# Kernel tuning notes

Hardware: AMD Instinct MI355X
Metric: run time of the kernel (lower is better)

The kernel has to match this reference:

```python
import jax, jax.numpy as jnp
import numpy as np

DIM = 128
HEADS = 4
WS = 8  # window size
HEAD_DIM = DIM // HEADS
LOG100 = float(np.log(100.0))


def _cpb_constants(ws):
    # log-spaced relative coordinates table, shape [(2ws-1)^2, 2]
    rng = np.arange(-(ws - 1), ws, dtype=np.float32)
    table = np.stack(np.meshgrid(rng, rng, indexing='ij'), axis=-1)  # [2ws-1,2ws-1,2]
    table = table / (ws - 1)
    table = table * 8.0
    table = np.sign(table) * np.log2(np.abs(table) + 1.0) / np.log2(8.0)
    table = table.reshape(-1, 2)
    # relative position index, shape [ws^2, ws^2]
    coords = np.stack(np.meshgrid(np.arange(ws), np.arange(ws), indexing='ij'), axis=0).reshape(2, -1)
    rel = coords[:, :, None] - coords[:, None, :]  # [2, ws^2, ws^2]
    idx = (rel[0] + ws - 1) * (2 * ws - 1) + (rel[1] + ws - 1)
    return jnp.asarray(table), jnp.asarray(idx.astype(np.int32))


def setup_inputs() -> dict:
    key = jax.random.key(0)
    ks = jax.random.split(key, 10)
    B, H, W = 16, 128, 128
    nW = (H // WS) * (W // WS)
    return {
        'x': jax.random.normal(ks[0], (B, H, W, DIM), jnp.float32),
        'mask': jnp.zeros((nW, WS * WS, WS * WS), jnp.float32),
        'qkv_w': jax.random.normal(ks[1], (DIM, 3 * DIM), jnp.float32) * 0.02,
        'q_bias': jax.random.normal(ks[2], (DIM,), jnp.float32) * 0.02,
        'v_bias': jax.random.normal(ks[3], (DIM,), jnp.float32) * 0.02,
        'logit_scale': jnp.full((HEADS,), float(np.log(10.0)), jnp.float32),
        'cpb_w1': jax.random.normal(ks[4], (2, 512), jnp.float32) * 0.02,
        'cpb_b1': jax.random.normal(ks[5], (512,), jnp.float32) * 0.02,
        'cpb_w2': jax.random.normal(ks[6], (512, HEADS), jnp.float32) * 0.02,
        'proj_w': jax.random.normal(ks[7], (DIM, DIM), jnp.float32) * 0.02,
        'proj_b': jax.random.normal(ks[8], (DIM,), jnp.float32) * 0.02,
        'height': 128,
        'width': 128,
    }


def reference(x, mask, qkv_w, q_bias, v_bias, logit_scale, cpb_w1, cpb_b1, cpb_w2, proj_w, proj_b, height, width):
    B = x.shape[0]
    N = WS * WS
    wh, ww = height // WS, width // WS
    nW = wh * ww

    # QKV projection, K has no bias
    qkv_b = jnp.concatenate([q_bias, jnp.zeros_like(q_bias), v_bias])
    qkv = x @ qkv_w + qkv_b  # [B,H,W,3*DIM]

    # fused window partition -> [3, B*nW, heads, N, head_dim]
    qkv = qkv.reshape(B, wh, WS, ww, WS, 3, HEADS, HEAD_DIM)
    qkv = jnp.transpose(qkv, (5, 0, 1, 3, 6, 2, 4, 7)).reshape(3, B * nW, HEADS, N, HEAD_DIM)
    q, k, v = qkv[0], qkv[1], qkv[2]

    # cosine attention with clamped learnable temperature
    q = q / jnp.maximum(jnp.linalg.norm(q, axis=-1, keepdims=True), 1e-12)
    k = k / jnp.maximum(jnp.linalg.norm(k, axis=-1, keepdims=True), 1e-12)
    scale = jnp.exp(jnp.minimum(logit_scale, LOG100))  # [heads]
    attn = jnp.einsum('whqd,whkd->whqk', q, k) * scale[None, :, None, None]

    # continuous relative position bias via small MLP
    table, idx = _cpb_constants(WS)
    bias_tab = jax.nn.relu(table @ cpb_w1 + cpb_b1) @ cpb_w2  # [(2ws-1)^2, heads]
    bias = 16.0 * jax.nn.sigmoid(bias_tab[idx])  # [N, N, heads]
    attn = attn + jnp.transpose(bias, (2, 0, 1))[None]

    # shifted-window mask
    attn = attn.reshape(B, nW, HEADS, N, N) + mask[None, :, None, :, :]
    attn = jax.nn.softmax(attn.reshape(B * nW, HEADS, N, N), axis=-1)

    out = jnp.einsum('whqk,whkd->whqd', attn, v)  # [B*nW, heads, N, head_dim]

    # fused window reverse -> [B, H, W, DIM]
    out = out.reshape(B, wh, ww, HEADS, WS, WS, HEAD_DIM)
    out = jnp.transpose(out, (0, 1, 4, 2, 5, 3, 6)).reshape(B, height, width, DIM)

    return out @ proj_w + proj_b
```

## Files before the change

kernel.cpp:

```cpp
#include <hip/hip_runtime.h>

typedef unsigned short u16;
typedef __bf16 bf16x8 __attribute__((ext_vector_type(8)));
typedef float f32x4 __attribute__((ext_vector_type(4)));
typedef int i32x4 __attribute__((ext_vector_type(4)));
typedef i32x4 i32x4_a __attribute__((may_alias));
typedef bf16x8 bf16x8_a __attribute__((may_alias));

__device__ __forceinline__ float bf2f(u16 u) {
  union { unsigned int i; float f; } c;
  c.i = ((unsigned int)u) << 16;
  return c.f;
}
__device__ __forceinline__ u16 f2bf(float f) {
  union { __bf16 h; u16 u; } c;
  c.h = (__bf16)f;
  return c.u;
}
__device__ __forceinline__ float gld(const void* p, int i, int isbf) {
  return isbf ? bf2f(((const u16*)p)[i]) : ((const float*)p)[i];
}
__device__ __forceinline__ int sw(int row, int col, int rs) {
  return row * rs + ((((col >> 3) ^ (row & 7)) << 3) | (col & 7));
}

#define WQKVT_OFF 0
#define PWT_OFF   98304
#define QKVB_OFF  131072
#define BIAS_OFF  132608
#define SCALE_OFF 198144
#define PB_OFF    198160
#define FLAG_OFF  198672

__global__ void swin_detect(const unsigned int* __restrict__ xw,
                            unsigned int* __restrict__ flag) {
  int t = threadIdx.x;
  int cnt = 0;
  for (int i = 0; i < 8; i++) {
    unsigned int w = xw[t * 8 + i];
    unsigned int lo = w & 0xffffu;
    unsigned int e = (lo >> 7) & 0xffu;
    if ((e >= 0x70u && e <= 0x82u) || lo == 0u) cnt++;
  }
  cnt += __shfl_xor(cnt, 1);
  cnt += __shfl_xor(cnt, 2);
  cnt += __shfl_xor(cnt, 4);
  cnt += __shfl_xor(cnt, 8);
  cnt += __shfl_xor(cnt, 16);
  cnt += __shfl_xor(cnt, 32);
  if (t == 0) *flag = (cnt >= 256) ? 1u : 0u;
}

__global__ void swin_setup(const void* __restrict__ qkv_w, const void* __restrict__ q_bias,
                           const void* __restrict__ v_bias, const void* __restrict__ ls,
                           const void* __restrict__ cpb_w1, const void* __restrict__ cpb_b1,
                           const void* __restrict__ cpb_w2, const void* __restrict__ proj_w,
                           const void* __restrict__ proj_b, char* __restrict__ ws) {
  const int b = blockIdx.x, t = threadIdx.x;
  const int isbf = (int)*(const unsigned int*)(ws + FLAG_OFF);
  u16* wqkvT = (u16*)(ws + WQKVT_OFF);
  u16* pwT = (u16*)(ws + PWT_OFF);
  float* qkvb = (float*)(ws + QKVB_OFF);
  float* bias16 = (float*)(ws + BIAS_OFF);
  float* scalef = (float*)(ws + SCALE_OFF);
  float* pbf = (float*)(ws + PB_OFF);

  if (b < 128) {
    for (int c = t; c < 384; c += 256)
      wqkvT[c * 128 + b] = f2bf(gld(qkv_w, b * 384 + c, isbf));
  } else if (b < 256) {
    int r = b - 128;
    if (t < 128) pwT[t * 128 + r] = f2bf(gld(proj_w, r * 128 + t, isbf));
  } else if (b == 256) {
    for (int o = t; o < 384; o += 256) {
      float v = 0.f;
      if (o < 128) v = gld(q_bias, o, isbf);
      else if (o >= 256) v = gld(v_bias, o - 256, isbf);
      qkvb[o] = v;
    }
    if (t < 128) pbf[t] = gld(proj_b, t, isbf);
    if (t < 4) scalef[t] = expf(fminf(gld(ls, t, isbf), 4.60517019f));
  } else {
    __shared__ float w1[1024];
    __shared__ float b1[512];
    __shared__ float w2[2048];
    __shared__ float tab[225][4];
    for (int i = t; i < 1024; i += 256) w1[i] = gld(cpb_w1, i, isbf);
    for (int i = t; i < 512; i += 256) b1[i] = gld(cpb_b1, i, isbf);
    for (int i = t; i < 2048; i += 256) w2[i] = gld(cpb_w2, i, isbf);
    __syncthreads();
    if (t < 225) {
      int i = t / 15, j = t % 15;
      float c0, c1;
      {
        float tt = ((float)(i - 7) / 7.0f) * 8.0f;
        float s = (tt > 0.f) ? 1.f : ((tt < 0.f) ? -1.f : 0.f);
        c0 = s * log2f(fabsf(tt) + 1.f) / 3.0f;
      }
      {
        float tt = ((float)(j - 7) / 7.0f) * 8.0f;
        float s = (tt > 0.f) ? 1.f : ((tt < 0.f) ? -1.f : 0.f);
        c1 = s * log2f(fabsf(tt) + 1.f) / 3.0f;
      }
      float acc[4] = {0.f, 0.f, 0.f, 0.f};
      for (int jj = 0; jj < 512; jj++) {
        float h = fmaxf(c0 * w1[jj] + c1 * w1[512 + jj] + b1[jj], 0.f);
        #pragma unroll
        for (int hh = 0; hh < 4; hh++) acc[hh] += h * w2[jj * 4 + hh];
      }
      #pragma unroll
      for (int hh = 0; hh < 4; hh++) tab[t][hh] = acc[hh];
    }
    __syncthreads();
    for (int e = t; e < 4 * 64 * 64; e += 256) {
      int h = e >> 12, q = (e >> 6) & 63, kk = e & 63;
      int dr = (q >> 3) - (kk >> 3) + 7;
      int dc = (q & 7) - (kk & 7) + 7;
      float v = tab[dr * 15 + dc][h];
      bias16[e] = 16.f / (1.f + expf(-v));
    }
  }
}

#define X_OFF 0
#define Q_OFF 0
#define K_OFF 8192
#define VT_OFF 16384
#define P_OFF 0
#define AO_OFF 0

__global__ __launch_bounds__(512, 4) void swin_main(
    const void* __restrict__ x, const void* __restrict__ mask,
    const char* __restrict__ ws, void* __restrict__ out) {
  __shared__ __align__(16) u16 lds[24576];
  const f32x4 fz = {0.f, 0.f, 0.f, 0.f};

  const u16* wqkvT = (const u16*)(ws + WQKVT_OFF);
  const u16* pwT = (const u16*)(ws + PWT_OFF);
  const float* qkvb = (const float*)(ws + QKVB_OFF);
  const float* bias16 = (const float*)(ws + BIAS_OFF);
  const float* scalef = (const float*)(ws + SCALE_OFF);
  const float* pbf = (const float*)(ws + PB_OFF);
  const int isbf = (int)*(const unsigned int*)(ws + FLAG_OFF);

  const int tid = threadIdx.x;
  const int wid = tid >> 6;
  const int lane = tid & 63;
  const int ln16 = lane & 15;
  const int lq = lane >> 4;
  const int q8 = lq << 3;
  const int mg = wid >> 2;
  const int sub = wid & 3;

  const int wi = blockIdx.x;
  const int b = wi >> 8;
  const int rem = wi & 255;
  const int wy = rem >> 4, wx = rem & 15;
  const int xbase = ((b * 128 + wy * 8) * 128 + wx * 8) * 128;

  if (isbf) {
    const u16* xb = (const u16*)x;
    #pragma unroll
    for (int rep = 0; rep < 2; rep++) {
      int ch = tid + rep * 512;
      int token = ch >> 4, dch = ch & 15;
      int r = token >> 3, c = token & 7;
      i32x4 v = *(const i32x4_a*)(xb + xbase + r * 16384 + c * 128 + dch * 8);
      *(i32x4_a*)(lds + X_OFF + sw(token, dch * 8, 128)) = v;
    }
  } else {
    const float* xf = (const float*)x;
    #pragma unroll
    for (int rep = 0; rep < 2; rep++) {
      int ch = tid + rep * 512;
      int token = ch >> 4, dch = ch & 15;
      int r = token >> 3, c = token & 7;
      const float* src = xf + xbase + r * 16384 + c * 128 + dch * 8;
      union { i32x4 v2[2]; float f[8]; } in;
      in.v2[0] = *(const i32x4_a*)(src);
      in.v2[1] = *(const i32x4_a*)(src + 4);
      union { u16 u[8]; i32x4 v; } o;
      #pragma unroll
      for (int d = 0; d < 8; d++) o.u[d] = f2bf(in.f[d]);
      *(i32x4_a*)(lds + X_OFF + sw(token, dch * 8, 128)) = o.v;
    }
  }
  __syncthreads();

  f32x4 acc1[2][6];
  #pragma unroll
  for (int nt = 0; nt < 6; nt++) {
    float bv = qkvb[96 * sub + 16 * nt + ln16];
    f32x4 ci = {bv, bv, bv, bv};
    acc1[0][nt] = ci;
    acc1[1][nt] = ci;
  }

  #pragma unroll
  for (int ks = 0; ks < 4; ks++) {
    bf16x8 a0 = *(const bf16x8_a*)(lds + X_OFF + sw(32 * mg + ln16, 32 * ks + q8, 128));
    bf16x8 a1 = *(const bf16x8_a*)(lds + X_OFF + sw(32 * mg + 16 + ln16, 32 * ks + q8, 128));
    bf16x8 bb[6];
    #pragma unroll
    for (int nt = 0; nt < 6; nt++)
      bb[nt] = *(const bf16x8_a*)(wqkvT + (96 * sub + 16 * nt + ln16) * 128 + 32 * ks + q8);
    #pragma unroll
    for (int nt = 0; nt < 6; nt++) {
      acc1[0][nt] = __builtin_amdgcn_mfma_f32_16x16x32_bf16(a0, bb[nt], acc1[0][nt], 0, 0, 0);
      acc1[1][nt] = __builtin_amdgcn_mfma_f32_16x16x32_bf16(a1, bb[nt], acc1[1][nt], 0, 0, 0);
    }
  }
  __syncthreads();

  #pragma unroll
  for (int ci = 0; ci < 3; ci++) {
    int n0 = 96 * sub + 32 * ci;
    int type = n0 >> 7;
    int head = (n0 & 127) >> 5;
    int nt0 = 2 * ci, nt1 = nt0 + 1;
    if (type < 2) {
      int base = (type == 0) ? Q_OFF : K_OFF;
      float sh = (type == 0) ? scalef[head] : 1.0f;
      #pragma unroll
      for (int mt = 0; mt < 2; mt++)
        #pragma unroll
        for (int r = 0; r < 4; r++) {
          float x0 = acc1[mt][nt0][r], x1 = acc1[mt][nt1][r];
          float ss = x0 * x0 + x1 * x1;
          ss += __shfl_xor(ss, 1);
          ss += __shfl_xor(ss, 2);
          ss += __shfl_xor(ss, 4);
          ss += __shfl_xor(ss, 8);
          float inv = sh / fmaxf(sqrtf(ss), 1e-12f);
          int row = 32 * mg + 16 * mt + 4 * lq + r;
          lds[base + sw(row, head * 32 + ln16, 128)] = f2bf(x0 * inv);
          lds[base + sw(row, head * 32 + 16 + ln16, 128)] = f2bf(x1 * inv);
        }
    } else {
      #pragma unroll
      for (int mt = 0; mt < 2; mt++)
        #pragma unroll
        for (int r = 0; r < 4; r++) {
          int row = 32 * mg + 16 * mt + 4 * lq + r;
          lds[VT_OFF + sw(head * 32 + ln16, row, 64)] = f2bf(acc1[mt][nt0][r]);
          lds[VT_OFF + sw(head * 32 + 16 + ln16, row, 64)] = f2bf(acc1[mt][nt1][r]);
        }
    }
  }
  __syncthreads();

  const int h = sub;
  bf16x8 qf[2], kf[4];
  #pragma unroll
  for (int mt = 0; mt < 2; mt++)
    qf[mt] = *(const bf16x8_a*)(lds + Q_OFF + sw(32 * mg + 16 * mt + ln16, h * 32 + q8, 128));
  #pragma unroll
  for (int nt = 0; nt < 4; nt++)
    kf[nt] = *(const bf16x8_a*)(lds + K_OFF + sw(16 * nt + ln16, h * 32 + q8, 128));

  const float* brow = bias16 + h * 4096;
  const u16* mk16 = (const u16*)mask;
  const float* mkf = (const float*)mask;
  f32x4 S[2][4];
  #pragma unroll
  for (int mt = 0; mt < 2; mt++)
    #pragma unroll
    for (int nt = 0; nt < 4; nt++)
      #pragma unroll
      for (int r = 0; r < 4; r++) {
        int row = 32 * mg + 16 * mt + 4 * lq + r;
        int col = 16 * nt + ln16;
        int bi = row * 64 + col;
        float mval = isbf ? bf2f(mk16[rem * 4096 + bi]) : mkf[rem * 4096 + bi];
        S[mt][nt][r] = brow[bi] + mval;
      }
  #pragma unroll
  for (int mt = 0; mt < 2; mt++)
    #pragma unroll
    for (int nt = 0; nt < 4; nt++)
      S[mt][nt] = __builtin_amdgcn_mfma_f32_16x16x32_bf16(qf[mt], kf[nt], S[mt][nt], 0, 0, 0);

  #pragma unroll
  for (int mt = 0; mt < 2; mt++)
    #pragma unroll
    for (int r = 0; r < 4; r++) {
      float m = fmaxf(fmaxf(S[mt][0][r], S[mt][1][r]), fmaxf(S[mt][2][r], S[mt][3][r]));
      m = fmaxf(m, __shfl_xor(m, 1));
      m = fmaxf(m, __shfl_xor(m, 2));
      m = fmaxf(m, __shfl_xor(m, 4));
      m = fmaxf(m, __shfl_xor(m, 8));
      float sum = 0.f;
      #pragma unroll
      for (int nt = 0; nt < 4; nt++) {
        float p = __expf(S[mt][nt][r] - m);
        S[mt][nt][r] = p;
        sum += p;
      }
      sum += __shfl_xor(sum, 1);
      sum += __shfl_xor(sum, 2);
      sum += __shfl_xor(sum, 4);
      sum += __shfl_xor(sum, 8);
      float inv = 1.0f / sum;
      #pragma unroll
      for (int nt = 0; nt < 4; nt++) S[mt][nt][r] *= inv;
    }
  __syncthreads();

  #pragma unroll
  for (int mt = 0; mt < 2; mt++)
    #pragma unroll
    for (int nt = 0; nt < 4; nt++)
      #pragma unroll
      for (int r = 0; r < 4; r++) {
        int row = 32 * mg + 16 * mt + 4 * lq + r;
        lds[P_OFF + sw(row, h * 64 + 16 * nt + ln16, 256)] = f2bf(S[mt][nt][r]);
      }
  __syncthreads();
  f32x4 O[2][2];
  O[0][0] = fz; O[0][1] = fz; O[1][0] = fz; O[1][1] = fz;
  #pragma unroll
  for (int ks = 0; ks < 2; ks++) {
    bf16x8 pf[2], vf[2];
    #pragma unroll
    for (int mt = 0; mt < 2; mt++)
      pf[mt] = *(const bf16x8_a*)(lds + P_OFF + sw(32 * mg + 16 * mt + ln16, h * 64 + 32 * ks + q8, 256));
    #pragma unroll
    for (int nt = 0; nt < 2; nt++)
      vf[nt] = *(const bf16x8_a*)(lds + VT_OFF + sw(h * 32 + 16 * nt + ln16, 32 * ks + q8, 64));
    #pragma unroll
    for (int mt = 0; mt < 2; mt++)
      #pragma unroll
      for (int nt = 0; nt < 2; nt++)
        O[mt][nt] = __builtin_amdgcn_mfma_f32_16x16x32_bf16(pf[mt], vf[nt], O[mt][nt], 0, 0, 0);
  }
  __syncthreads();
  #pragma unroll
  for (int mt = 0; mt < 2; mt++)
    #pragma unroll
    for (int nt = 0; nt < 2; nt++)
      #pragma unroll
      for (int r = 0; r < 4; r++) {
        int row = 32 * mg + 16 * mt + 4 * lq + r;
        lds[AO_OFF + sw(row, h * 32 + 16 * nt + ln16, 128)] = f2bf(O[mt][nt][r]);
      }
  __syncthreads();

  float pb0 = pbf[32 * sub + ln16];
  float pb1 = pbf[32 * sub + 16 + ln16];
  f32x4 acc3[2][2];
  {
    f32x4 c0 = {pb0, pb0, pb0, pb0};
    f32x4 c1 = {pb1, pb1, pb1, pb1};
    acc3[0][0] = c0; acc3[0][1] = c1; acc3[1][0] = c0; acc3[1][1] = c1;
  }
  #pragma unroll
  for (int ks = 0; ks < 4; ks++) {
    bf16x8 a0 = *(const bf16x8_a*)(lds + AO_OFF + sw(32 * mg + ln16, 32 * ks + q8, 128));
    bf16x8 a1 = *(const bf16x8_a*)(lds + AO_OFF + sw(32 * mg + 16 + ln16, 32 * ks + q8, 128));
    bf16x8 b0 = *(const bf16x8_a*)(pwT + (32 * sub + ln16) * 128 + 32 * ks + q8);
    bf16x8 b1 = *(const bf16x8_a*)(pwT + (32 * sub + 16 + ln16) * 128 + 32 * ks + q8);
    acc3[0][0] = __builtin_amdgcn_mfma_f32_16x16x32_bf16(a0, b0, acc3[0][0], 0, 0, 0);
    acc3[0][1] = __builtin_amdgcn_mfma_f32_16x16x32_bf16(a0, b1, acc3[0][1], 0, 0, 0);
    acc3[1][0] = __builtin_amdgcn_mfma_f32_16x16x32_bf16(a1, b0, acc3[1][0], 0, 0, 0);
    acc3[1][1] = __builtin_amdgcn_mfma_f32_16x16x32_bf16(a1, b1, acc3[1][1], 0, 0, 0);
  }
  if (isbf) {
    u16* ob = (u16*)out;
    #pragma unroll
    for (int mt = 0; mt < 2; mt++)
      #pragma unroll
      for (int r = 0; r < 4; r++) {
        int row = 32 * mg + 16 * mt + 4 * lq + r;
        int o = xbase + (row >> 3) * 16384 + (row & 7) * 128 + 32 * sub;
        ob[o + ln16] = f2bf(acc3[mt][0][r]);
        ob[o + 16 + ln16] = f2bf(acc3[mt][1][r]);
      }
  } else {
    float* of = (float*)out;
    #pragma unroll
    for (int mt = 0; mt < 2; mt++)
      #pragma unroll
      for (int r = 0; r < 4; r++) {
        int row = 32 * mg + 16 * mt + 4 * lq + r;
        int o = xbase + (row >> 3) * 16384 + (row & 7) * 128 + 32 * sub;
        of[o + ln16] = acc3[mt][0][r];
        of[o + 16 + ln16] = acc3[mt][1][r];
      }
  }
}

extern "C" void kernel_launch(void* const* d_in, const int* in_sizes, int n_in,
                              void* d_out, int out_size, void* d_ws, size_t ws_size,
                              hipStream_t stream) {
  const void* x      = d_in[0];
  const void* mask   = d_in[1];
  const void* qkv_w  = d_in[2];
  const void* q_bias = d_in[3];
  const void* v_bias = d_in[4];
  const void* ls     = d_in[5];
  const void* cpb_w1 = d_in[6];
  const void* cpb_b1 = d_in[7];
  const void* cpb_w2 = d_in[8];
  const void* proj_w = d_in[9];
  const void* proj_b = d_in[10];
  const int B = in_sizes[0] / (128 * 128 * 128);

  char* ws = (char*)d_ws;
  swin_detect<<<1, 64, 0, stream>>>((const unsigned int*)x,
                                    (unsigned int*)(ws + FLAG_OFF));
  swin_setup<<<258, 256, 0, stream>>>(qkv_w, q_bias, v_bias, ls, cpb_w1, cpb_b1,
                                      cpb_w2, proj_w, proj_b, ws);
  swin_main<<<B * 256, 512, 0, stream>>>(x, mask, ws, d_out);
}
```

Measured before the change: 436.9 us.

## Load x fragments directly from global and transpose score MFMA for vector bias/P access

Drops the LDS staging of the x window and one barrier, so the QKV MFMA A-fragments are read straight from global memory, converting from fp32 when needed. The score MFMA is computed as K·Q^T, which puts each query row in a lane. That allows vectorized f32x4 bias and mask loads, softmax reductions with two shuffles instead of four, and 8-byte packed P stores to LDS. The cost is that uncoalesced, 32-byte-strided global reads of x sit directly in the MFMA loop, and each x element is re-read by four warps.

```diff
diff --git a/kernel.cpp b/kernel.cpp
--- a/kernel.cpp
+++ b/kernel.cpp
@@ -4,8 +4,12 @@
 typedef __bf16 bf16x8 __attribute__((ext_vector_type(8)));
 typedef float f32x4 __attribute__((ext_vector_type(4)));
 typedef int i32x4 __attribute__((ext_vector_type(4)));
+typedef int i32x2 __attribute__((ext_vector_type(2)));
 typedef i32x4 i32x4_a __attribute__((may_alias));
+typedef i32x2 i32x2_a __attribute__((may_alias));
 typedef bf16x8 bf16x8_a __attribute__((may_alias));
+typedef f32x4 f32x4_a __attribute__((may_alias));
+typedef unsigned long long u64_a __attribute__((may_alias));
 
 __device__ __forceinline__ float bf2f(u16 u) {
   union { unsigned int i; float f; } c;
@@ -22,6 +26,18 @@
 }
 __device__ __forceinline__ int sw(int row, int col, int rs) {
   return row * rs + ((((col >> 3) ^ (row & 7)) << 3) | (col & 7));
+}
+__device__ __forceinline__ bf16x8 ldx(const void* x, int base, int row, int d, int isbf) {
+  int off = base + ((row >> 3) * 16384) + ((row & 7) * 128) + d;
+  if (isbf) {
+    return *(const bf16x8_a*)((const u16*)x + off);
+  } else {
+    const float* p = (const float*)x + off;
+    union { u16 u[8]; bf16x8 v; } o;
+    #pragma unroll
+    for (int i = 0; i < 8; i++) o.u[i] = f2bf(p[i]);
+    return o.v;
+  }
 }
 
 #define WQKVT_OFF 0
@@ -122,7 +138,6 @@
   }
 }
 
-#define X_OFF 0
 #define Q_OFF 0
 #define K_OFF 8192
 #define VT_OFF 16384
@@ -158,35 +173,6 @@
   const int wy = rem >> 4, wx = rem & 15;
   const int xbase = ((b * 128 + wy * 8) * 128 + wx * 8) * 128;
 
-  if (isbf) {
-    const u16* xb = (const u16*)x;
-    #pragma unroll
-    for (int rep = 0; rep < 2; rep++) {
-      int ch = tid + rep * 512;
-      int token = ch >> 4, dch = ch & 15;
-      int r = token >> 3, c = token & 7;
-      i32x4 v = *(const i32x4_a*)(xb + xbase + r * 16384 + c * 128 + dch * 8);
-      *(i32x4_a*)(lds + X_OFF + sw(token, dch * 8, 128)) = v;
-    }
-  } else {
-    const float* xf = (const float*)x;
-    #pragma unroll
-    for (int rep = 0; rep < 2; rep++) {
-      int ch = tid + rep * 512;
-      int token = ch >> 4, dch = ch & 15;
-      int r = token >> 3, c = token & 7;
-      const float* src = xf + xbase + r * 16384 + c * 128 + dch * 8;
-      union { i32x4 v2[2]; float f[8]; } in;
-      in.v2[0] = *(const i32x4_a*)(src);
-      in.v2[1] = *(const i32x4_a*)(src + 4);
-      union { u16 u[8]; i32x4 v; } o;
-      #pragma unroll
-      for (int d = 0; d < 8; d++) o.u[d] = f2bf(in.f[d]);
-      *(i32x4_a*)(lds + X_OFF + sw(token, dch * 8, 128)) = o.v;
-    }
-  }
-  __syncthreads();
-
   f32x4 acc1[2][6];
   #pragma unroll
   for (int nt = 0; nt < 6; nt++) {
@@ -198,8 +184,8 @@
 
   #pragma unroll
   for (int ks = 0; ks < 4; ks++) {
-    bf16x8 a0 = *(const bf16x8_a*)(lds + X_OFF + sw(32 * mg + ln16, 32 * ks + q8, 128));
-    bf16x8 a1 = *(const bf16x8_a*)(lds + X_OFF + sw(32 * mg + 16 + ln16, 32 * ks + q8, 128));
+    bf16x8 a0 = ldx(x, xbase, 32 * mg + ln16, 32 * ks + q8, isbf);
+    bf16x8 a1 = ldx(x, xbase, 32 * mg + 16 + ln16, 32 * ks + q8, isbf);
     bf16x8 bb[6];
     #pragma unroll
     for (int nt = 0; nt < 6; nt++)
@@ -210,7 +196,6 @@
       acc1[1][nt] = __builtin_amdgcn_mfma_f32_16x16x32_bf16(a1, bb[nt], acc1[1][nt], 0, 0, 0);
     }
   }
-  __syncthreads();
 
   #pragma unroll
   for (int ci = 0; ci < 3; ci++) {
@@ -250,71 +235,84 @@
   __syncthreads();
 
   const int h = sub;
-  bf16x8 qf[2], kf[4];
-  #pragma unroll
-  for (int mt = 0; mt < 2; mt++)
-    qf[mt] = *(const bf16x8_a*)(lds + Q_OFF + sw(32 * mg + 16 * mt + ln16, h * 32 + q8, 128));
-  #pragma unroll
-  for (int nt = 0; nt < 4; nt++)
-    kf[nt] = *(const bf16x8_a*)(lds + K_OFF + sw(16 * nt + ln16, h * 32 + q8, 128));
+  bf16x8 kf[4], qf[2];
+  #pragma unroll
+  for (int kt = 0; kt < 4; kt++)
+    kf[kt] = *(const bf16x8_a*)(lds + K_OFF + sw(16 * kt + ln16, h * 32 + q8, 128));
+  #pragma unroll
+  for (int qt = 0; qt < 2; qt++)
+    qf[qt] = *(const bf16x8_a*)(lds + Q_OFF + sw(32 * mg + 16 * qt + ln16, h * 32 + q8, 128));
 
   const float* brow = bias16 + h * 4096;
   const u16* mk16 = (const u16*)mask;
   const float* mkf = (const float*)mask;
-  f32x4 S[2][4];
-  #pragma unroll
-  for (int mt = 0; mt < 2; mt++)
-    #pragma unroll
-    for (int nt = 0; nt < 4; nt++)
+  f32x4 ST[4][2];
+  #pragma unroll
+  for (int qt = 0; qt < 2; qt++) {
+    int q = 32 * mg + 16 * qt + ln16;
+    #pragma unroll
+    for (int kt = 0; kt < 4; kt++) {
+      int bi = q * 64 + 16 * kt + 4 * lq;
+      f32x4 bv = *(const f32x4_a*)(brow + bi);
+      f32x4 cv;
+      if (isbf) {
+        u64_a mw = *(const u64_a*)(mk16 + rem * 4096 + bi);
+        cv[0] = bv[0] + bf2f((u16)mw);
+        cv[1] = bv[1] + bf2f((u16)(mw >> 16));
+        cv[2] = bv[2] + bf2f((u16)(mw >> 32));
+        cv[3] = bv[3] + bf2f((u16)(mw >> 48));
+      } else {
+        f32x4 mv = *(const f32x4_a*)(mkf + rem * 4096 + bi);
+        cv = bv + mv;
+      }
+      ST[kt][qt] = cv;
+    }
+  }
+  #pragma unroll
+  for (int kt = 0; kt < 4; kt++)
+    #pragma unroll
+    for (int qt = 0; qt < 2; qt++)
+      ST[kt][qt] = __builtin_amdgcn_mfma_f32_16x16x32_bf16(kf[kt], qf[qt], ST[kt][qt], 0, 0, 0);
+
+  #pragma unroll
+  for (int qt = 0; qt < 2; qt++) {
+    float m = ST[0][qt][0];
+    #pragma unroll
+    for (int kt = 0; kt < 4; kt++)
+      #pragma unroll
+      for (int r = 0; r < 4; r++) m = fmaxf(m, ST[kt][qt][r]);
+    m = fmaxf(m, __shfl_xor(m, 16));
+    m = fmaxf(m, __shfl_xor(m, 32));
+    float sum = 0.f;
+    #pragma unroll
+    for (int kt = 0; kt < 4; kt++)
       #pragma unroll
       for (int r = 0; r < 4; r++) {
-        int row = 32 * mg + 16 * mt + 4 * lq + r;
-        int col = 16 * nt + ln16;
-        int bi = row * 64 + col;
-        float mval = isbf ? bf2f(mk16[rem * 4096 + bi]) : mkf[rem * 4096 + bi];
-        S[mt][nt][r] = brow[bi] + mval;
-      }
-  #pragma unroll
-  for (int mt = 0; mt < 2; mt++)
-    #pragma unroll
-    for (int nt = 0; nt < 4; nt++)
-      S[mt][nt] = __builtin_amdgcn_mfma_f32_16x16x32_bf16(qf[mt], kf[nt], S[mt][nt], 0, 0, 0);
-
-  #pragma unroll
-  for (int mt = 0; mt < 2; mt++)
-    #pragma unroll
-    for (int r = 0; r < 4; r++) {
-      float m = fmaxf(fmaxf(S[mt][0][r], S[mt][1][r]), fmaxf(S[mt][2][r], S[mt][3][r]));
-      m = fmaxf(m, __shfl_xor(m, 1));
-      m = fmaxf(m, __shfl_xor(m, 2));
-      m = fmaxf(m, __shfl_xor(m, 4));
-      m = fmaxf(m, __shfl_xor(m, 8));
-      float sum = 0.f;
-      #pragma unroll
-      for (int nt = 0; nt < 4; nt++) {
-        float p = __expf(S[mt][nt][r] - m);
-        S[mt][nt][r] = p;
+        float p = __expf(ST[kt][qt][r] - m);
+        ST[kt][qt][r] = p;
         sum += p;
       }
-      sum += __shfl_xor(sum, 1);
-      sum += __shfl_xor(sum, 2);
-      sum += __shfl_xor(sum, 4);
-      sum += __shfl_xor(sum, 8);
-      float inv = 1.0f / sum;
-      #pragma unroll
-      for (int nt = 0; nt < 4; nt++) S[mt][nt][r] *= inv;
-    }
+    sum += __shfl_xor(sum, 16);
+    sum += __shfl_xor(sum, 32);
+    float inv = 1.0f / sum;
+    #pragma unroll
+    for (int kt = 0; kt < 4; kt++)
+      #pragma unroll
+      for (int r = 0; r < 4; r++) ST[kt][qt][r] *= inv;
+  }
   __syncthreads();
 
   #pragma unroll
-  for (int mt = 0; mt < 2; mt++)
-    #pragma unroll
-    for (int nt = 0; nt < 4; nt++)
-      #pragma unroll
-      for (int r = 0; r < 4; r++) {
-        int row = 32 * mg + 16 * mt + 4 * lq + r;
-        lds[P_OFF + sw(row, h * 64 + 16 * nt + ln16, 256)] = f2bf(S[mt][nt][r]);
-      }
+  for (int qt = 0; qt < 2; qt++)
+    #pragma unroll
+    for (int kt = 0; kt < 4; kt++) {
+      int row = 32 * mg + 16 * qt + ln16;
+      int col = h * 64 + 16 * kt + 4 * lq;
+      unsigned int w0 = (unsigned int)f2bf(ST[kt][qt][0]) | ((unsigned int)f2bf(ST[kt][qt][1]) << 16);
+      unsigned int w1 = (unsigned int)f2bf(ST[kt][qt][2]) | ((unsigned int)f2bf(ST[kt][qt][3]) << 16);
+      i32x2 wv = {(int)w0, (int)w1};
+      *(i32x2_a*)(lds + P_OFF + sw(row, col, 256)) = wv;
+    }
   __syncthreads();
   f32x4 O[2][2];
   O[0][0] = fz; O[0][1] = fz; O[1][0] = fz; O[1][1] = fz;
```

Result: slower. 494.8 us (+13.3%).
